# Optimization experiments

Measured on AMD Instinct MI355X. Metric: run time of the kernel, lower is better.

Reference implementation:

```python
import jax, jax.numpy as jnp
import numpy as np

B, L, D, K, NRBF = 2, 2048, 128, 3, 16
NUM_ATOMS = 118


def setup_inputs() -> dict:
    key = jax.random.key(0)
    ks = jax.random.split(key, 20)
    s = 0.05
    inp = {
        "coords": jax.random.normal(ks[0], (B, L, 3), dtype=jnp.float32) * 3.0,
        "Z": jax.random.randint(ks[1], (B, L), 0, NUM_ATOMS),
        # CoordEncoder params
        "atom_emb": jax.random.normal(ks[2], (NUM_ATOMS, D), dtype=jnp.float32) * s,
        "gamma": jnp.asarray(10.0, dtype=jnp.float32),
        "rbf_centers": jnp.linspace(0.0, 5.0, NRBF, dtype=jnp.float32),
        "rbf_w": jax.random.normal(ks[3], (NRBF, D), dtype=jnp.float32) * s,
        "rbf_b": jnp.zeros((D,), dtype=jnp.float32),
        "out_w": jax.random.normal(ks[4], (2 * D, D), dtype=jnp.float32) * s,
        "out_b": jnp.zeros((D,), dtype=jnp.float32),
        # MP_Layer params, stacked over K layers
        "self_w": jax.random.normal(ks[5], (K, D, D), dtype=jnp.float32) * s,
        "self_b": jnp.zeros((K, D), dtype=jnp.float32),
        "msg_w": jax.random.normal(ks[6], (K, D, D), dtype=jnp.float32) * s,
        "msg_b": jnp.zeros((K, D), dtype=jnp.float32),
        "upd_w": jax.random.normal(ks[7], (K, 2 * D, D), dtype=jnp.float32) * s,
        "upd_b": jnp.zeros((K, D), dtype=jnp.float32),
    }
    return inp


def _pairwise_dist(coords):
    # coords: [B,L,3] -> dist: [B,L,L]; safe sqrt so diagonal has zero grad
    diff = coords[:, :, None, :] - coords[:, None, :, :]
    sq = jnp.sum(diff * diff, axis=-1)
    return jnp.where(sq > 0, jnp.sqrt(jnp.where(sq > 0, sq, 1.0)), 0.0)


def reference(coords, Z, atom_emb, gamma, rbf_centers, rbf_w, rbf_b,
              out_w, out_b, self_w, self_b, msg_w, msg_b, upd_w, upd_b):
    # --- CoordEncoder ---
    h_atom = atom_emb[Z]                                   # [B,L,D]
    dist = _pairwise_dist(coords)                          # [B,L,L]
    rbf = jnp.exp(-gamma * (dist[..., None] - rbf_centers) ** 2)  # [B,L,L,R]
    rbf_local = rbf.mean(axis=2)                           # [B,L,R]
    h_geo = rbf_local @ rbf_w + rbf_b                      # [B,L,D]
    h = jnp.concatenate([h_atom, h_geo], axis=-1) @ out_w + out_b  # [B,L,D]
    # --- MP layers (mask is None; W = exp(-dist) is the same every layer) ---
    W = jnp.exp(-dist)                                     # [B,L,L]
    for k in range(K):
        msg = jnp.einsum("bij,bjd->bid", W, h @ msg_w[k] + msg_b[k])
        h = jnp.concatenate([h @ self_w[k] + self_b[k], msg], axis=-1) @ upd_w[k] + upd_b[k]
    return h
```

## Files before the change

kernel.cpp:

```cpp
#include <hip/hip_runtime.h>
#include <hip/hip_bf16.h>

typedef unsigned short u16;
typedef __bf16 bf16x8 __attribute__((ext_vector_type(8)));
typedef float f32x4 __attribute__((ext_vector_type(4)));
typedef u16 u16x4 __attribute__((ext_vector_type(4)));

#define B_ 2
#define L_ 2048
#define D_ 128
#define KLAY 3
#define NR 16
#define NATOM 118
#define DD (D_ * D_)
#define XTN (L_ * D_)

static __device__ __forceinline__ u16 f2bf(float f) {
    union { float f; unsigned u; } v; v.f = f;
    unsigned r = v.u + 0x7FFFu + ((v.u >> 16) & 1u);
    return (u16)(r >> 16);
}
static __device__ __forceinline__ bf16x8 ld_bf8(const u16* p) {
    return *(const bf16x8*)p;
}

__global__ __launch_bounds__(256) void prep_kernel(
    const float* atom_emb, const float* out_w, const float* self_w,
    const float* msg_w, const float* upd_w,
    u16* atom16, u16* outwT, u16* selfT, u16* msgT, u16* updT) {
    const int T0 = NATOM * D_;
    const int T1 = D_ * 2 * D_;
    const int T2 = KLAY * DD;
    const int T3 = KLAY * DD;
    const int T4 = KLAY * 2 * DD;
    int total = T0 + T1 + T2 + T3 + T4;
    for (int t = blockIdx.x * blockDim.x + threadIdx.x; t < total;
         t += gridDim.x * blockDim.x) {
        int u = t;
        if (u < T0) { atom16[u] = f2bf(atom_emb[u]); continue; }
        u -= T0;
        if (u < T1) {
            int n = u / (2 * D_), k = u % (2 * D_);
            outwT[u] = f2bf(out_w[k * D_ + n]);
            continue;
        }
        u -= T1;
        if (u < T2) {
            int kk = u / DD, v = u % DD;
            int n = v / D_, k = v % D_;
            selfT[u] = f2bf(self_w[kk * DD + k * D_ + n]);
            continue;
        }
        u -= T2;
        if (u < T3) {
            int kk = u / DD, v = u % DD;
            int n = v / D_, k = v % D_;
            msgT[u] = f2bf(msg_w[kk * DD + k * D_ + n]);
            continue;
        }
        u -= T3;
        {
            int kk = u / (2 * DD), v = u % (2 * DD);
            int n = v / (2 * D_), k = v % (2 * D_);
            updT[u] = f2bf(upd_w[kk * 2 * DD + k * D_ + n]);
        }
    }
}

__global__ __launch_bounds__(256) void rbf_kernel(
    const float* coords, const float* gamma_p, const float* centers,
    float* rbf_loc) {
    int w = threadIdx.x >> 6, lane = threadIdx.x & 63;
    int bi = blockIdx.x * 4 + w;
    int b = bi >> 11;
    float gamma = gamma_p[0];
    float dl = centers[1] - centers[0];
    float c4[4];
#pragma unroll
    for (int g = 0; g < 4; g++) c4[g] = centers[4 * g];
    float two_gdl = 2.f * gamma * dl;
    float cx = coords[bi * 3 + 0];
    float cy = coords[bi * 3 + 1];
    float cz = coords[bi * 3 + 2];
    const float* cb = coords + (size_t)b * L_ * 3;
    float acc[4][4];
#pragma unroll
    for (int g = 0; g < 4; g++)
#pragma unroll
        for (int m = 0; m < 4; m++) acc[g][m] = 0.f;
    for (int it = 0; it < L_ / 64; it++) {
        int j = lane + 64 * it;
        float dx = cx - cb[j * 3 + 0];
        float dy = cy - cb[j * 3 + 1];
        float dz = cz - cb[j * 3 + 2];
        float sq = dx * dx + dy * dy + dz * dz;
        float d = sq > 0.f ? sqrtf(sq) : 0.f;
#pragma unroll
        for (int g = 0; g < 4; g++) {
            float x = d - c4[g];
            float base = __expf(-gamma * x * x);
            float u = __expf(fminf(two_gdl * x, 29.f));
            float p = base;
            acc[g][0] += p;
            p *= u; acc[g][1] += p;
            p *= u; acc[g][2] += p;
            p *= u; acc[g][3] += p;
        }
    }
#pragma unroll
    for (int off = 32; off > 0; off >>= 1)
#pragma unroll
        for (int g = 0; g < 4; g++)
#pragma unroll
            for (int m = 0; m < 4; m++) acc[g][m] += __shfl_xor(acc[g][m], off);
    if (lane == 0) {
#pragma unroll
        for (int m = 0; m < 4; m++) {
            float Km = __expf(-gamma * (m * dl) * (m * dl)) * (1.0f / L_);
#pragma unroll
            for (int g = 0; g < 4; g++)
                rbf_loc[(size_t)bi * NR + 4 * g + m] = acc[g][m] * Km;
        }
    }
}

__global__ __launch_bounds__(256) void enc_sx_kernel(
    const int* Z, const float* rbf_w, const float* rbf_b, const float* out_b,
    const float* rbf_loc, const u16* atom16, const u16* outwT,
    const u16* selfT0, const u16* msgT0, const float* self_b0, const float* msg_b0,
    u16* S16, u16* XT16) {
    int gi0 = blockIdx.x * 16;
    int b = gi0 >> 11;
    int il0 = gi0 & (L_ - 1);
    int tid = threadIdx.x;
    __shared__ __align__(16) u16 hgeo[16][136];
    __shared__ __align__(16) u16 h_lds[16][136];
    for (int e = tid; e < 16 * D_; e += 256) {
        int row = e >> 7, d = e & 127;
        int gi = gi0 + row;
        float s = rbf_b[d];
#pragma unroll
        for (int r = 0; r < NR; r++)
            s += rbf_loc[(size_t)gi * NR + r] * rbf_w[r * D_ + d];
        hgeo[row][d] = f2bf(s);
    }
    __syncthreads();
    int w = tid >> 6, lane = tid & 63;
    int rowf = lane & 15, kg = lane >> 4;
    f32x4 z = {0.f, 0.f, 0.f, 0.f};
    f32x4 acc[2] = {z, z};
    int za = Z[gi0 + rowf];
    for (int ks = 0; ks < 8; ks++) {
        int k0 = ks * 32 + kg * 8;
        bf16x8 a;
        if (k0 < 128) a = ld_bf8(atom16 + za * D_ + k0);
        else a = ld_bf8(&hgeo[rowf][k0 - 128]);
#pragma unroll
        for (int q = 0; q < 2; q++) {
            int cl = (w * 2 + q) * 16 + rowf;
            bf16x8 bb = ld_bf8(outwT + cl * (2 * D_) + k0);
            acc[q] = __builtin_amdgcn_mfma_f32_16x16x32_bf16(a, bb, acc[q], 0, 0, 0);
        }
    }
#pragma unroll
    for (int q = 0; q < 2; q++) {
        int cl = (w * 2 + q) * 16 + rowf;
        float bias = out_b[cl];
#pragma unroll
        for (int r = 0; r < 4; r++) h_lds[kg * 4 + r][cl] = f2bf(acc[q][r] + bias);
    }
    __syncthreads();
    f32x4 acc3[4] = {z, z, z, z};
    for (int ks = 0; ks < 4; ks++) {
        int k0 = ks * 32 + kg * 8;
        bf16x8 a = ld_bf8(&h_lds[rowf][k0]);
#pragma unroll
        for (int q = 0; q < 4; q++) {
            int nb = w * 4 + q;
            const u16* wp = (nb < 8) ? (selfT0 + (nb * 16 + rowf) * D_ + k0)
                                     : (msgT0 + ((nb - 8) * 16 + rowf) * D_ + k0);
            acc3[q] = __builtin_amdgcn_mfma_f32_16x16x32_bf16(a, ld_bf8(wp), acc3[q], 0, 0, 0);
        }
    }
#pragma unroll
    for (int q = 0; q < 4; q++) {
        int nb = w * 4 + q;
        if (nb < 8) {
            int cl = nb * 16 + rowf;
            float bias = self_b0[cl];
#pragma unroll
            for (int r = 0; r < 4; r++)
                S16[(size_t)(gi0 + kg * 4 + r) * D_ + cl] = f2bf(acc3[q][r] + bias);
        } else {
            int cl = (nb - 8) * 16 + rowf;
            float bias = msg_b0[cl];
            u16x4 pk;
#pragma unroll
            for (int r = 0; r < 4; r++) pk[r] = f2bf(acc3[q][r] + bias);
            int jj = il0 + kg * 4;
            *(u16x4*)(XT16 + (size_t)b * XTN + (jj >> 5) * (32 * D_) + cl * 32 + (jj & 31)) = pk;
        }
    }
}

__global__ __launch_bounds__(512, 2) void mp_fused_kernel(
    const float* coords, const u16* XT_in, const u16* S_in,
    const u16* updT_k, const float* upd_b_k,
    const u16* selfTn, const u16* msgTn, const float* self_bn, const float* msg_bn,
    u16* S_out, u16* XT_out, float* out_f32, int last) {
    int gi0 = blockIdx.x * 16;
    int b = gi0 >> 11;
    int il0 = gi0 & (L_ - 1);
    int tid = threadIdx.x;
    int w = tid >> 6, lane = tid & 63;
    int rowf = lane & 15, kg = lane >> 4;

    __shared__ __align__(16) float red[4][16][128];
    __shared__ __align__(16) float cj[L_ * 3];
    u16* msg_lds = (u16*)&red[0][0][0];
    u16* h_lds = (u16*)&red[1][0][0];

    {
        const float4* src = (const float4*)(coords + (size_t)b * L_ * 3);
        float4* dst = (float4*)cj;
#pragma unroll
        for (int i = 0; i < 3; i++) dst[tid + i * 512] = src[tid + i * 512];
    }
    __syncthreads();

    float rx = cj[(il0 + rowf) * 3 + 0];
    float ry = cj[(il0 + rowf) * 3 + 1];
    float rz = cj[(il0 + rowf) * 3 + 2];

    f32x4 z = {0.f, 0.f, 0.f, 0.f};
    f32x4 acc[8] = {z, z, z, z, z, z, z, z};
    const u16* xbase = XT_in + (size_t)b * XTN + (w * 8) * (32 * D_) + rowf * 32 + kg * 8;
#pragma unroll
    for (int s = 0; s < 8; s++) {
        int j0 = w * 256 + s * 32 + kg * 8;
        const float* jc = &cj[j0 * 3];
        union { bf16x8 v; __bf16 e[8]; } wf;
#pragma unroll
        for (int e = 0; e < 8; e++) {
            float dx = rx - jc[e * 3 + 0];
            float dy = ry - jc[e * 3 + 1];
            float dz = rz - jc[e * 3 + 2];
            float sq = dx * dx + dy * dy + dz * dz;
            float d = sq > 0.f ? sqrtf(sq) : 0.f;
            wf.e[e] = (__bf16)__expf(-d);
        }
#pragma unroll
        for (int n = 0; n < 8; n++) {
            bf16x8 bb = ld_bf8(xbase + s * (32 * D_) + n * 512);
            acc[n] = __builtin_amdgcn_mfma_f32_16x16x32_bf16(wf.v, bb, acc[n], 0, 0, 0);
        }
    }
    auto stash = [&](int slot) {
#pragma unroll
        for (int n = 0; n < 8; n++)
#pragma unroll
            for (int r = 0; r < 4; r++) {
                int row = kg * 4 + r, col = n * 16 + rowf;
                red[slot][row][(col + 4 * row) & 127] = acc[n][r];
            }
    };
    auto grab = [&](int slot) {
#pragma unroll
        for (int n = 0; n < 8; n++)
#pragma unroll
            for (int r = 0; r < 4; r++) {
                int row = kg * 4 + r, col = n * 16 + rowf;
                acc[n][r] += red[slot][row][(col + 4 * row) & 127];
            }
    };
    if (w >= 4) stash(w - 4);
    __syncthreads();
    if (w < 4) grab(w);
    if (w == 2 || w == 3) stash(w);
    __syncthreads();
    if (w < 2) grab(w + 2);
    if (w == 1) stash(3);
    __syncthreads();
    if (w == 0) {
        grab(3);
#pragma unroll
        for (int n = 0; n < 8; n++)
#pragma unroll
            for (int r = 0; r < 4; r++)
                msg_lds[(kg * 4 + r) * 136 + n * 16 + rowf] = f2bf(acc[n][r]);
    }
    __syncthreads();
    f32x4 acc2 = z;
    int cl = w * 16 + rowf;
#pragma unroll
    for (int ks = 0; ks < 8; ks++) {
        int k0 = ks * 32 + kg * 8;
        bf16x8 av = (ks < 4) ? ld_bf8(S_in + (size_t)(gi0 + rowf) * D_ + k0)
                             : ld_bf8(msg_lds + rowf * 136 + (k0 - 128));
        acc2 = __builtin_amdgcn_mfma_f32_16x16x32_bf16(
            av, ld_bf8(updT_k + cl * 2 * D_ + k0), acc2, 0, 0, 0);
    }
    float bias = upd_b_k[cl];
    if (last) {
#pragma unroll
        for (int r = 0; r < 4; r++)
            out_f32[(size_t)(gi0 + kg * 4 + r) * D_ + cl] = acc2[r] + bias;
        return;
    }
#pragma unroll
    for (int r = 0; r < 4; r++)
        h_lds[(kg * 4 + r) * 136 + cl] = f2bf(acc2[r] + bias);
    __syncthreads();
    f32x4 a30 = z, a31 = z;
#pragma unroll
    for (int ks = 0; ks < 4; ks++) {
        int k0 = ks * 32 + kg * 8;
        bf16x8 av = ld_bf8(h_lds + rowf * 136 + k0);
        a30 = __builtin_amdgcn_mfma_f32_16x16x32_bf16(
            av, ld_bf8(selfTn + cl * D_ + k0), a30, 0, 0, 0);
        a31 = __builtin_amdgcn_mfma_f32_16x16x32_bf16(
            av, ld_bf8(msgTn + cl * D_ + k0), a31, 0, 0, 0);
    }
    float bs = self_bn[cl], bm = msg_bn[cl];
#pragma unroll
    for (int r = 0; r < 4; r++)
        S_out[(size_t)(gi0 + kg * 4 + r) * D_ + cl] = f2bf(a30[r] + bs);
    u16x4 pk;
#pragma unroll
    for (int r = 0; r < 4; r++) pk[r] = f2bf(a31[r] + bm);
    int jj = il0 + kg * 4;
    *(u16x4*)(XT_out + (size_t)b * XTN + (jj >> 5) * (32 * D_) + cl * 32 + (jj & 31)) = pk;
}

extern "C" void kernel_launch(void* const* d_in, const int* in_sizes, int n_in,
                              void* d_out, int out_size, void* d_ws, size_t ws_size,
                              hipStream_t stream) {
    const float* coords = (const float*)d_in[0];
    const int* Z = (const int*)d_in[1];
    const float* atom_emb = (const float*)d_in[2];
    const float* gamma = (const float*)d_in[3];
    const float* centers = (const float*)d_in[4];
    const float* rbf_w = (const float*)d_in[5];
    const float* rbf_b = (const float*)d_in[6];
    const float* out_w = (const float*)d_in[7];
    const float* out_b = (const float*)d_in[8];
    const float* self_w = (const float*)d_in[9];
    const float* self_b = (const float*)d_in[10];
    const float* msg_w = (const float*)d_in[11];
    const float* msg_b = (const float*)d_in[12];
    const float* upd_w = (const float*)d_in[13];
    const float* upd_b = (const float*)d_in[14];
    float* out = (float*)d_out;

    char* ws = (char*)d_ws;
    u16* S_a = (u16*)(ws + 0);
    u16* S_b = (u16*)(ws + 1048576);
    u16* XT_a = (u16*)(ws + 2097152);
    u16* XT_b = (u16*)(ws + 3145728);
    float* rbfl = (float*)(ws + 4194304);
    u16* atom16 = (u16*)(ws + 4456448);
    u16* outwT = (u16*)(ws + 4489216);
    u16* selfT = (u16*)(ws + 4554752);
    u16* msgT = (u16*)(ws + 4653056);
    u16* updT = (u16*)(ws + 4751360);

    prep_kernel<<<64, 256, 0, stream>>>(atom_emb, out_w, self_w, msg_w, upd_w,
                                        atom16, outwT, selfT, msgT, updT);
    rbf_kernel<<<(B_ * L_) / 4, 256, 0, stream>>>(coords, gamma, centers, rbfl);
    enc_sx_kernel<<<(B_ * L_) / 16, 256, 0, stream>>>(
        Z, rbf_w, rbf_b, out_b, rbfl, atom16, outwT,
        selfT, msgT, self_b, msg_b, S_a, XT_a);
    mp_fused_kernel<<<256, 512, 0, stream>>>(
        coords, XT_a, S_a, updT + 0 * 2 * DD, upd_b + 0 * D_,
        selfT + 1 * DD, msgT + 1 * DD, self_b + 1 * D_, msg_b + 1 * D_,
        S_b, XT_b, out, 0);
    mp_fused_kernel<<<256, 512, 0, stream>>>(
        coords, XT_b, S_b, updT + 1 * 2 * DD, upd_b + 1 * D_,
        selfT + 2 * DD, msgT + 2 * DD, self_b + 2 * D_, msg_b + 2 * D_,
        S_a, XT_a, out, 0);
    mp_fused_kernel<<<256, 512, 0, stream>>>(
        coords, XT_a, S_a, updT + 2 * 2 * DD, upd_b + 2 * D_,
        selfT, msgT, self_b, msg_b, S_b, XT_b, out, 1);
}
```

Measured before the change: 108.1 us.

## Precompute bf16 exp(-dist) weight matrix once and reuse across MP layers

The RBF pass now also writes the pairwise weight matrix W=exp(-dist) as bf16 in MFMA fragment layout to workspace (16 MB). The three message-passing kernels load it instead of recomputing distances and exponentials per layer. The RBF kernel is split over four column quarters with partial sums reduced in the encoder kernel, which gives more blocks. This trades repeated sqrt/exp ALU work for extra global memory traffic to write and read W, which can be partly served from cache.

```diff
diff --git a/kernel.cpp b/kernel.cpp
--- a/kernel.cpp
+++ b/kernel.cpp
@@ -14,6 +14,7 @@
 #define NATOM 118
 #define DD (D_ * D_)
 #define XTN (L_ * D_)
+#define BLN (B_ * L_ * NR)
 
 static __device__ __forceinline__ u16 f2bf(float f) {
     union { float f; unsigned u; } v; v.f = f;
@@ -67,34 +68,50 @@
     }
 }
 
-__global__ __launch_bounds__(256) void rbf_kernel(
+__global__ __launch_bounds__(512) void pairw_kernel(
     const float* coords, const float* gamma_p, const float* centers,
-    float* rbf_loc) {
-    int w = threadIdx.x >> 6, lane = threadIdx.x & 63;
-    int bi = blockIdx.x * 4 + w;
-    int b = bi >> 11;
+    u16* Wf, float* rbfp) {
+    int bid = blockIdx.x;
+    int rt = bid >> 2, jq = bid & 3;
+    int gi0 = rt * 16;
+    int b = gi0 >> 11;
+    int t = threadIdx.x;
+    int row = t >> 5, k = t & 31;
+    int gi = gi0 + row;
+
+    __shared__ float cj[512 * 3];
+    {
+        const float4* src = (const float4*)(coords + ((size_t)b * L_ + jq * 512) * 3);
+        float4* dst = (float4*)cj;
+        if (t < 384) dst[t] = src[t];
+    }
     float gamma = gamma_p[0];
     float dl = centers[1] - centers[0];
     float c4[4];
 #pragma unroll
     for (int g = 0; g < 4; g++) c4[g] = centers[4 * g];
     float two_gdl = 2.f * gamma * dl;
-    float cx = coords[bi * 3 + 0];
-    float cy = coords[bi * 3 + 1];
-    float cz = coords[bi * 3 + 2];
-    const float* cb = coords + (size_t)b * L_ * 3;
+    float cx = coords[gi * 3 + 0];
+    float cy = coords[gi * 3 + 1];
+    float cz = coords[gi * 3 + 2];
+    __syncthreads();
+
     float acc[4][4];
 #pragma unroll
     for (int g = 0; g < 4; g++)
 #pragma unroll
         for (int m = 0; m < 4; m++) acc[g][m] = 0.f;
-    for (int it = 0; it < L_ / 64; it++) {
-        int j = lane + 64 * it;
-        float dx = cx - cb[j * 3 + 0];
-        float dy = cy - cb[j * 3 + 1];
-        float dz = cz - cb[j * 3 + 2];
+
+    u16* wbase = Wf + (size_t)rt * (64 * 512) + (jq * 16) * 512 + t;
+#pragma unroll 4
+    for (int s = 0; s < 16; s++) {
+        int jl = s * 32 + k;
+        float dx = cx - cj[jl * 3 + 0];
+        float dy = cy - cj[jl * 3 + 1];
+        float dz = cz - cj[jl * 3 + 2];
         float sq = dx * dx + dy * dy + dz * dz;
-        float d = sq > 0.f ? sqrtf(sq) : 0.f;
+        float d = sqrtf(sq);
+        wbase[s * 512] = f2bf(__expf(-d));
 #pragma unroll
         for (int g = 0; g < 4; g++) {
             float x = d - c4[g];
@@ -108,40 +125,48 @@
         }
     }
 #pragma unroll
-    for (int off = 32; off > 0; off >>= 1)
+    for (int off = 16; off > 0; off >>= 1)
 #pragma unroll
         for (int g = 0; g < 4; g++)
 #pragma unroll
             for (int m = 0; m < 4; m++) acc[g][m] += __shfl_xor(acc[g][m], off);
-    if (lane == 0) {
+    if (k == 0) {
 #pragma unroll
         for (int m = 0; m < 4; m++) {
             float Km = __expf(-gamma * (m * dl) * (m * dl)) * (1.0f / L_);
 #pragma unroll
             for (int g = 0; g < 4; g++)
-                rbf_loc[(size_t)bi * NR + 4 * g + m] = acc[g][m] * Km;
+                rbfp[(size_t)jq * BLN + (size_t)gi * NR + 4 * g + m] = acc[g][m] * Km;
         }
     }
 }
 
 __global__ __launch_bounds__(256) void enc_sx_kernel(
     const int* Z, const float* rbf_w, const float* rbf_b, const float* out_b,
-    const float* rbf_loc, const u16* atom16, const u16* outwT,
+    const float* rbfp, const u16* atom16, const u16* outwT,
     const u16* selfT0, const u16* msgT0, const float* self_b0, const float* msg_b0,
     u16* S16, u16* XT16) {
     int gi0 = blockIdx.x * 16;
     int b = gi0 >> 11;
     int il0 = gi0 & (L_ - 1);
     int tid = threadIdx.x;
+    __shared__ float rbf_lds[16][NR];
     __shared__ __align__(16) u16 hgeo[16][136];
     __shared__ __align__(16) u16 h_lds[16][136];
+    {
+        int row = tid >> 4, r = tid & 15;
+        float s = 0.f;
+#pragma unroll
+        for (int p = 0; p < 4; p++)
+            s += rbfp[(size_t)p * BLN + (size_t)(gi0 + row) * NR + r];
+        rbf_lds[row][r] = s;
+    }
+    __syncthreads();
     for (int e = tid; e < 16 * D_; e += 256) {
         int row = e >> 7, d = e & 127;
-        int gi = gi0 + row;
         float s = rbf_b[d];
 #pragma unroll
-        for (int r = 0; r < NR; r++)
-            s += rbf_loc[(size_t)gi * NR + r] * rbf_w[r * D_ + d];
+        for (int r = 0; r < NR; r++) s += rbf_lds[row][r] * rbf_w[r * D_ + d];
         hgeo[row][d] = f2bf(s);
     }
     __syncthreads();
@@ -204,11 +229,12 @@
 }
 
 __global__ __launch_bounds__(512, 2) void mp_fused_kernel(
-    const float* coords, const u16* XT_in, const u16* S_in,
+    const u16* Wf, const u16* XT_in, const u16* S_in,
     const u16* updT_k, const float* upd_b_k,
     const u16* selfTn, const u16* msgTn, const float* self_bn, const float* msg_bn,
     u16* S_out, u16* XT_out, float* out_f32, int last) {
-    int gi0 = blockIdx.x * 16;
+    int rt = blockIdx.x;
+    int gi0 = rt * 16;
     int b = gi0 >> 11;
     int il0 = gi0 & (L_ - 1);
     int tid = threadIdx.x;
@@ -216,43 +242,20 @@
     int rowf = lane & 15, kg = lane >> 4;
 
     __shared__ __align__(16) float red[4][16][128];
-    __shared__ __align__(16) float cj[L_ * 3];
     u16* msg_lds = (u16*)&red[0][0][0];
     u16* h_lds = (u16*)&red[1][0][0];
 
-    {
-        const float4* src = (const float4*)(coords + (size_t)b * L_ * 3);
-        float4* dst = (float4*)cj;
-#pragma unroll
-        for (int i = 0; i < 3; i++) dst[tid + i * 512] = src[tid + i * 512];
-    }
-    __syncthreads();
-
-    float rx = cj[(il0 + rowf) * 3 + 0];
-    float ry = cj[(il0 + rowf) * 3 + 1];
-    float rz = cj[(il0 + rowf) * 3 + 2];
-
     f32x4 z = {0.f, 0.f, 0.f, 0.f};
     f32x4 acc[8] = {z, z, z, z, z, z, z, z};
+    const u16* abase = Wf + (size_t)rt * (64 * 512) + (w * 8) * 512 + rowf * 32 + kg * 8;
     const u16* xbase = XT_in + (size_t)b * XTN + (w * 8) * (32 * D_) + rowf * 32 + kg * 8;
 #pragma unroll
     for (int s = 0; s < 8; s++) {
-        int j0 = w * 256 + s * 32 + kg * 8;
-        const float* jc = &cj[j0 * 3];
-        union { bf16x8 v; __bf16 e[8]; } wf;
-#pragma unroll
-        for (int e = 0; e < 8; e++) {
-            float dx = rx - jc[e * 3 + 0];
-            float dy = ry - jc[e * 3 + 1];
-            float dz = rz - jc[e * 3 + 2];
-            float sq = dx * dx + dy * dy + dz * dz;
-            float d = sq > 0.f ? sqrtf(sq) : 0.f;
-            wf.e[e] = (__bf16)__expf(-d);
-        }
+        bf16x8 a = ld_bf8(abase + s * 512);
 #pragma unroll
         for (int n = 0; n < 8; n++) {
             bf16x8 bb = ld_bf8(xbase + s * (32 * D_) + n * 512);
-            acc[n] = __builtin_amdgcn_mfma_f32_16x16x32_bf16(wf.v, bb, acc[n], 0, 0, 0);
+            acc[n] = __builtin_amdgcn_mfma_f32_16x16x32_bf16(a, bb, acc[n], 0, 0, 0);
         }
     }
     auto stash = [&](int slot) {
@@ -353,32 +356,34 @@
     float* out = (float*)d_out;
 
     char* ws = (char*)d_ws;
-    u16* S_a = (u16*)(ws + 0);
-    u16* S_b = (u16*)(ws + 1048576);
-    u16* XT_a = (u16*)(ws + 2097152);
-    u16* XT_b = (u16*)(ws + 3145728);
-    float* rbfl = (float*)(ws + 4194304);
-    u16* atom16 = (u16*)(ws + 4456448);
-    u16* outwT = (u16*)(ws + 4489216);
-    u16* selfT = (u16*)(ws + 4554752);
-    u16* msgT = (u16*)(ws + 4653056);
-    u16* updT = (u16*)(ws + 4751360);
+    u16* Wf = (u16*)(ws + 0);
+    u16* S_a = (u16*)(ws + 16777216);
+    u16* S_b = (u16*)(ws + 17825792);
+    u16* XT_a = (u16*)(ws + 18874368);
+    u16* XT_b = (u16*)(ws + 19922944);
+    float* rbfp = (float*)(ws + 20971520);
+    u16* atom16 = (u16*)(ws + 22020096);
+    u16* outwT = (u16*)(ws + 22052864);
+    u16* selfT = (u16*)(ws + 22118400);
+    u16* msgT = (u16*)(ws + 22216704);
+    u16* updT = (u16*)(ws + 22315008);
 
     prep_kernel<<<64, 256, 0, stream>>>(atom_emb, out_w, self_w, msg_w, upd_w,
                                         atom16, outwT, selfT, msgT, updT);
-    rbf_kernel<<<(B_ * L_) / 4, 256, 0, stream>>>(coords, gamma, centers, rbfl);
+    pairw_kernel<<<(B_ * L_ / 16) * 4, 512, 0, stream>>>(coords, gamma, centers,
+                                                         Wf, rbfp);
     enc_sx_kernel<<<(B_ * L_) / 16, 256, 0, stream>>>(
-        Z, rbf_w, rbf_b, out_b, rbfl, atom16, outwT,
+        Z, rbf_w, rbf_b, out_b, rbfp, atom16, outwT,
         selfT, msgT, self_b, msg_b, S_a, XT_a);
     mp_fused_kernel<<<256, 512, 0, stream>>>(
-        coords, XT_a, S_a, updT + 0 * 2 * DD, upd_b + 0 * D_,
+        Wf, XT_a, S_a, updT + 0 * 2 * DD, upd_b + 0 * D_,
         selfT + 1 * DD, msgT + 1 * DD, self_b + 1 * D_, msg_b + 1 * D_,
         S_b, XT_b, out, 0);
     mp_fused_kernel<<<256, 512, 0, stream>>>(
-        coords, XT_b, S_b, updT + 1 * 2 * DD, upd_b + 1 * D_,
+        Wf, XT_b, S_b, updT + 1 * 2 * DD, upd_b + 1 * D_,
         selfT + 2 * DD, msgT + 2 * DD, self_b + 2 * D_, msg_b + 2 * D_,
         S_a, XT_a, out, 0);
     mp_fused_kernel<<<256, 512, 0, stream>>>(
-        coords, XT_a, S_a, updT + 2 * 2 * DD, upd_b + 2 * D_,
+        Wf, XT_a, S_a, updT + 2 * 2 * DD, upd_b + 2 * D_,
         selfT, msgT, self_b, msg_b, S_b, XT_b, out, 1);
 }
```

New measurement: 121.9 us. +12.8%, slower.

## Restructure MP kernel to 1024 threads with LDS-staged W tiles and column-split waves

Applied to the files above, without the earlier changes.

Rewrites the fused message-passing kernel so 16 waves each own a 16-column slice and half of the neighbor range. Distance weights are computed once per block into LDS in chunks of 1024 neighbors and shared by all waves. This replaces the eight-accumulator, multi-step cross-wave reduction with a single two-way reduction, and spreads the self/msg projections across all waves. It adds LDS traffic for W, extra barriers per chunk, and a larger block size that may limit occupancy.

```diff
diff --git a/kernel.cpp b/kernel.cpp
--- a/kernel.cpp
+++ b/kernel.cpp
@@ -14,6 +14,7 @@
 #define NATOM 118
 #define DD (D_ * D_)
 #define XTN (L_ * D_)
+#define CHUNK 1024
 
 static __device__ __forceinline__ u16 f2bf(float f) {
     union { float f; unsigned u; } v; v.f = f;
@@ -203,133 +204,128 @@
     }
 }
 
-__global__ __launch_bounds__(512, 2) void mp_fused_kernel(
+__global__ __launch_bounds__(1024, 4) void mp_fused_kernel(
     const float* coords, const u16* XT_in, const u16* S_in,
     const u16* updT_k, const float* upd_b_k,
     const u16* selfTn, const u16* msgTn, const float* self_bn, const float* msg_bn,
     u16* S_out, u16* XT_out, float* out_f32, int last) {
-    int gi0 = blockIdx.x * 16;
+    int rt = blockIdx.x;
+    int gi0 = rt * 16;
     int b = gi0 >> 11;
     int il0 = gi0 & (L_ - 1);
     int tid = threadIdx.x;
     int w = tid >> 6, lane = tid & 63;
     int rowf = lane & 15, kg = lane >> 4;
 
-    __shared__ __align__(16) float red[4][16][128];
-    __shared__ __align__(16) float cj[L_ * 3];
-    u16* msg_lds = (u16*)&red[0][0][0];
-    u16* h_lds = (u16*)&red[1][0][0];
-
+    __shared__ float cj[CHUNK * 3];
+    __shared__ __align__(16) u16 Wlds[32][4][16][8];
+    __shared__ float red[8][16][20];
+    __shared__ __align__(16) u16 msg_lds[16][136];
+    __shared__ __align__(16) u16 h_lds[16][136];
+
+    int grow = tid & 15, jg = tid >> 4;
+    float rx = coords[(gi0 + grow) * 3 + 0];
+    float ry = coords[(gi0 + grow) * 3 + 1];
+    float rz = coords[(gi0 + grow) * 3 + 2];
+
+    int nb = w & 7, jh = w >> 3;
+    f32x4 z = {0.f, 0.f, 0.f, 0.f};
+    f32x4 acc = z;
+
+    for (int c = 0; c < 2; c++) {
+        if (tid < CHUNK * 3 / 4) {
+            ((float4*)cj)[tid] =
+                ((const float4*)(coords + ((size_t)b * L_ + c * CHUNK) * 3))[tid];
+        }
+        __syncthreads();
+#pragma unroll
+        for (int it = 0; it < 2; it++) {
+            int j0 = it * 512 + jg * 8;
+            union { bf16x8 v; u16 e[8]; } pk;
+#pragma unroll
+            for (int e = 0; e < 8; e++) {
+                int jl = j0 + e;
+                float dx = rx - cj[jl * 3 + 0];
+                float dy = ry - cj[jl * 3 + 1];
+                float dz = rz - cj[jl * 3 + 2];
+                float sq = dx * dx + dy * dy + dz * dz;
+                float d = sqrtf(sq);
+                pk.e[e] = f2bf(__expf(-d));
+            }
+            *(bf16x8*)&Wlds[j0 >> 5][(j0 & 31) >> 3][grow][0] = pk.v;
+        }
+        __syncthreads();
+        const u16* xb = XT_in + (size_t)b * XTN + (c * 32 + jh * 16) * (32 * D_) +
+                        (nb * 16 + rowf) * 32 + kg * 8;
+#pragma unroll
+        for (int si = 0; si < 16; si++) {
+            bf16x8 a = *(const bf16x8*)&Wlds[jh * 16 + si][kg][rowf][0];
+            bf16x8 bb = ld_bf8(xb + si * (32 * D_));
+            acc = __builtin_amdgcn_mfma_f32_16x16x32_bf16(a, bb, acc, 0, 0, 0);
+        }
+        __syncthreads();
+    }
+    if (jh == 1) {
+#pragma unroll
+        for (int r = 0; r < 4; r++) red[nb][kg * 4 + r][rowf] = acc[r];
+    }
+    __syncthreads();
+    if (jh == 0) {
+#pragma unroll
+        for (int r = 0; r < 4; r++) {
+            float m = acc[r] + red[nb][kg * 4 + r][rowf];
+            msg_lds[kg * 4 + r][nb * 16 + rowf] = f2bf(m);
+        }
+    }
+    __syncthreads();
+    if (w < 8) {
+        f32x4 acc2 = z;
+        int cl = w * 16 + rowf;
+#pragma unroll
+        for (int ks = 0; ks < 8; ks++) {
+            int k0 = ks * 32 + kg * 8;
+            bf16x8 av = (ks < 4) ? ld_bf8(S_in + (size_t)(gi0 + rowf) * D_ + k0)
+                                 : ld_bf8(&msg_lds[rowf][k0 - 128]);
+            acc2 = __builtin_amdgcn_mfma_f32_16x16x32_bf16(
+                av, ld_bf8(updT_k + cl * 2 * D_ + k0), acc2, 0, 0, 0);
+        }
+        float bias = upd_b_k[cl];
+        if (last) {
+#pragma unroll
+            for (int r = 0; r < 4; r++)
+                out_f32[(size_t)(gi0 + kg * 4 + r) * D_ + cl] = acc2[r] + bias;
+        } else {
+#pragma unroll
+            for (int r = 0; r < 4; r++)
+                h_lds[kg * 4 + r][cl] = f2bf(acc2[r] + bias);
+        }
+    }
+    if (last) return;
+    __syncthreads();
     {
-        const float4* src = (const float4*)(coords + (size_t)b * L_ * 3);
-        float4* dst = (float4*)cj;
-#pragma unroll
-        for (int i = 0; i < 3; i++) dst[tid + i * 512] = src[tid + i * 512];
-    }
-    __syncthreads();
-
-    float rx = cj[(il0 + rowf) * 3 + 0];
-    float ry = cj[(il0 + rowf) * 3 + 1];
-    float rz = cj[(il0 + rowf) * 3 + 2];
-
-    f32x4 z = {0.f, 0.f, 0.f, 0.f};
-    f32x4 acc[8] = {z, z, z, z, z, z, z, z};
-    const u16* xbase = XT_in + (size_t)b * XTN + (w * 8) * (32 * D_) + rowf * 32 + kg * 8;
-#pragma unroll
-    for (int s = 0; s < 8; s++) {
-        int j0 = w * 256 + s * 32 + kg * 8;
-        const float* jc = &cj[j0 * 3];
-        union { bf16x8 v; __bf16 e[8]; } wf;
-#pragma unroll
-        for (int e = 0; e < 8; e++) {
-            float dx = rx - jc[e * 3 + 0];
-            float dy = ry - jc[e * 3 + 1];
-            float dz = rz - jc[e * 3 + 2];
-            float sq = dx * dx + dy * dy + dz * dz;
-            float d = sq > 0.f ? sqrtf(sq) : 0.f;
-            wf.e[e] = (__bf16)__expf(-d);
-        }
-#pragma unroll
-        for (int n = 0; n < 8; n++) {
-            bf16x8 bb = ld_bf8(xbase + s * (32 * D_) + n * 512);
-            acc[n] = __builtin_amdgcn_mfma_f32_16x16x32_bf16(wf.v, bb, acc[n], 0, 0, 0);
-        }
-    }
-    auto stash = [&](int slot) {
-#pragma unroll
-        for (int n = 0; n < 8; n++)
-#pragma unroll
-            for (int r = 0; r < 4; r++) {
-                int row = kg * 4 + r, col = n * 16 + rowf;
-                red[slot][row][(col + 4 * row) & 127] = acc[n][r];
-            }
-    };
-    auto grab = [&](int slot) {
-#pragma unroll
-        for (int n = 0; n < 8; n++)
-#pragma unroll
-            for (int r = 0; r < 4; r++) {
-                int row = kg * 4 + r, col = n * 16 + rowf;
-                acc[n][r] += red[slot][row][(col + 4 * row) & 127];
-            }
-    };
-    if (w >= 4) stash(w - 4);
-    __syncthreads();
-    if (w < 4) grab(w);
-    if (w == 2 || w == 3) stash(w);
-    __syncthreads();
-    if (w < 2) grab(w + 2);
-    if (w == 1) stash(3);
-    __syncthreads();
-    if (w == 0) {
-        grab(3);
-#pragma unroll
-        for (int n = 0; n < 8; n++)
+        int cl = nb * 16 + rowf;
+        const u16* wT = (w < 8) ? (selfTn + cl * D_) : (msgTn + cl * D_);
+        f32x4 a3 = z;
+#pragma unroll
+        for (int ks = 0; ks < 4; ks++) {
+            int k0 = ks * 32 + kg * 8;
+            a3 = __builtin_amdgcn_mfma_f32_16x16x32_bf16(
+                ld_bf8(&h_lds[rowf][k0]), ld_bf8(wT + k0), a3, 0, 0, 0);
+        }
+        if (w < 8) {
+            float bias = self_bn[cl];
 #pragma unroll
             for (int r = 0; r < 4; r++)
-                msg_lds[(kg * 4 + r) * 136 + n * 16 + rowf] = f2bf(acc[n][r]);
-    }
-    __syncthreads();
-    f32x4 acc2 = z;
-    int cl = w * 16 + rowf;
-#pragma unroll
-    for (int ks = 0; ks < 8; ks++) {
-        int k0 = ks * 32 + kg * 8;
-        bf16x8 av = (ks < 4) ? ld_bf8(S_in + (size_t)(gi0 + rowf) * D_ + k0)
-                             : ld_bf8(msg_lds + rowf * 136 + (k0 - 128));
-        acc2 = __builtin_amdgcn_mfma_f32_16x16x32_bf16(
-            av, ld_bf8(updT_k + cl * 2 * D_ + k0), acc2, 0, 0, 0);
-    }
-    float bias = upd_b_k[cl];
-    if (last) {
-#pragma unroll
-        for (int r = 0; r < 4; r++)
-            out_f32[(size_t)(gi0 + kg * 4 + r) * D_ + cl] = acc2[r] + bias;
-        return;
-    }
-#pragma unroll
-    for (int r = 0; r < 4; r++)
-        h_lds[(kg * 4 + r) * 136 + cl] = f2bf(acc2[r] + bias);
-    __syncthreads();
-    f32x4 a30 = z, a31 = z;
-#pragma unroll
-    for (int ks = 0; ks < 4; ks++) {
-        int k0 = ks * 32 + kg * 8;
-        bf16x8 av = ld_bf8(h_lds + rowf * 136 + k0);
-        a30 = __builtin_amdgcn_mfma_f32_16x16x32_bf16(
-            av, ld_bf8(selfTn + cl * D_ + k0), a30, 0, 0, 0);
-        a31 = __builtin_amdgcn_mfma_f32_16x16x32_bf16(
-            av, ld_bf8(msgTn + cl * D_ + k0), a31, 0, 0, 0);
-    }
-    float bs = self_bn[cl], bm = msg_bn[cl];
-#pragma unroll
-    for (int r = 0; r < 4; r++)
-        S_out[(size_t)(gi0 + kg * 4 + r) * D_ + cl] = f2bf(a30[r] + bs);
-    u16x4 pk;
-#pragma unroll
-    for (int r = 0; r < 4; r++) pk[r] = f2bf(a31[r] + bm);
-    int jj = il0 + kg * 4;
-    *(u16x4*)(XT_out + (size_t)b * XTN + (jj >> 5) * (32 * D_) + cl * 32 + (jj & 31)) = pk;
+                S_out[(size_t)(gi0 + kg * 4 + r) * D_ + cl] = f2bf(a3[r] + bias);
+        } else {
+            float bias = msg_bn[cl];
+            u16x4 pk;
+#pragma unroll
+            for (int r = 0; r < 4; r++) pk[r] = f2bf(a3[r] + bias);
+            int jj = il0 + kg * 4;
+            *(u16x4*)(XT_out + (size_t)b * XTN + (jj >> 5) * (32 * D_) + cl * 32 + (jj & 31)) = pk;
+        }
+    }
 }
 
 extern "C" void kernel_launch(void* const* d_in, const int* in_sizes, int n_in,
@@ -370,15 +366,15 @@
     enc_sx_kernel<<<(B_ * L_) / 16, 256, 0, stream>>>(
         Z, rbf_w, rbf_b, out_b, rbfl, atom16, outwT,
         selfT, msgT, self_b, msg_b, S_a, XT_a);
-    mp_fused_kernel<<<256, 512, 0, stream>>>(
+    mp_fused_kernel<<<256, 1024, 0, stream>>>(
         coords, XT_a, S_a, updT + 0 * 2 * DD, upd_b + 0 * D_,
         selfT + 1 * DD, msgT + 1 * DD, self_b + 1 * D_, msg_b + 1 * D_,
         S_b, XT_b, out, 0);
-    mp_fused_kernel<<<256, 512, 0, stream>>>(
+    mp_fused_kernel<<<256, 1024, 0, stream>>>(
         coords, XT_b, S_b, updT + 1 * 2 * DD, upd_b + 1 * D_,
         selfT + 2 * DD, msgT + 2 * DD, self_b + 2 * D_, msg_b + 2 * D_,
         S_a, XT_a, out, 0);
-    mp_fused_kernel<<<256, 512, 0, stream>>>(
+    mp_fused_kernel<<<256, 1024, 0, stream>>>(
         coords, XT_a, S_a, updT + 2 * 2 * DD, upd_b + 2 * D_,
         selfT, msgT, self_b, msg_b, S_b, XT_b, out, 1);
 }
```

After: 109.1 us. Within noise of the previous version (+0.9%).
